# Optimization experiments

Hardware: AMD Instinct MI355X
Metric: run time of the kernel (lower is better)

The kernel has to match this reference:

```python
import jax, jax.numpy as jnp
import numpy as np

TAU = 1.2       # LIF membrane time constant
VTH = 0.5       # spike threshold
ALPHA = 4.0     # spikingjelly default sigmoid surrogate sharpness


def setup_inputs() -> dict:
    key = jax.random.key(0)
    ks = jax.random.split(key, 14)
    T, B, C, L = 4, 16, 256, 2048

    def lin_w(k, o, i):
        return (jax.random.normal(k, (o, i), jnp.float32) / np.sqrt(i)).astype(jnp.float32)

    def bias(k, o):
        return (jax.random.normal(k, (o,), jnp.float32) * 0.01).astype(jnp.float32)

    return {
        "x": jax.random.normal(ks[0], (T, B, C, L), jnp.float32),
        "diffusion_step": jax.random.randint(ks[1], (B,), 0, 50),
        # diffusion_embedding: Linear(1,C) -> SiLU -> Linear(C,C)
        "w_emb1": lin_w(ks[2], C, 1), "b_emb1": bias(ks[3], C),
        "w_emb2": lin_w(ks[4], C, C), "b_emb2": bias(ks[5], C),
        # diffusion_projection: Linear(C,C)
        "w_proj": lin_w(ks[6], C, C), "b_proj": bias(ks[7], C),
        # conv: Conv1d(C, 2C, k=3, pad=1)
        "w_conv": (jax.random.normal(ks[8], (2 * C, C, 3), jnp.float32) / np.sqrt(3 * C)).astype(jnp.float32),
        "b_conv": bias(ks[9], 2 * C),
        # skip_out / res_out: Conv1d(C, C, k=1)
        "w_skip": (jax.random.normal(ks[10], (C, C, 1), jnp.float32) / np.sqrt(C)).astype(jnp.float32),
        "b_skip": bias(ks[11], C),
        "w_res": (jax.random.normal(ks[12], (C, C, 1), jnp.float32) / np.sqrt(C)).astype(jnp.float32),
        "b_res": bias(ks[13], C),
    }


def _heaviside_surrogate(u):
    # forward: (u >= 0); backward: sigmoid surrogate (spikingjelly default)
    s = jax.nn.sigmoid(ALPHA * u)
    return s + jax.lax.stop_gradient((u >= 0).astype(u.dtype) - s)


def _lif_multistep(x_seq):
    # x_seq: (T, B, C2, L); hard reset to v_reset=0, detach_reset=True
    def step(v, xt):
        v = v + (xt - v) / TAU                      # decay_input charging
        spike = _heaviside_surrogate(v - VTH)
        v = v * (1.0 - jax.lax.stop_gradient(spike))  # detached hard reset
        return v, spike

    v0 = jnp.zeros(x_seq.shape[1:], x_seq.dtype)
    _, spikes = jax.lax.scan(step, v0, x_seq)
    return spikes


def reference(x, diffusion_step, w_emb1, b_emb1, w_emb2, b_emb2, w_proj, b_proj,
              w_conv, b_conv, w_skip, b_skip, w_res, b_res):
    T, B, C, L = x.shape
    ds = diffusion_step.reshape(B, 1).astype(jnp.float32)
    h = jax.nn.silu(ds @ w_emb1.T + b_emb1)           # (B, C)
    emb = h @ w_emb2.T + b_emb2                       # (B, C)
    proj = emb @ w_proj.T + b_proj                    # (B, C)

    y = x + proj[None, :, :, None]                    # broadcast over T, L

    # Conv1d over flattened (T*B) batch, C -> 2C, k=3, pad=1
    y2 = jax.lax.conv_general_dilated(
        y.reshape(T * B, C, L), w_conv, window_strides=(1,),
        padding=[(1, 1)], rhs_dilation=(1,),
        dimension_numbers=("NCH", "OIH", "NCH"))
    y2 = (y2 + b_conv[None, :, None]).reshape(T, B, 2 * C, L)

    spikes = _lif_multistep(y2)                       # (T, B, 2C, L) in {0,1}

    gate, filt = spikes[:, :, :C, :], spikes[:, :, C:, :]
    z = jax.nn.sigmoid(gate) * jnp.tanh(filt)         # (T, B, C, L)

    skip = jnp.einsum("tbcl,oc->tbol", z, w_skip[:, :, 0]) + b_skip[None, None, :, None]
    res = jnp.einsum("tbcl,oc->tbol", z, w_res[:, :, 0]) + b_res[None, None, :, None]
    return (x + res, skip)
```

## Files before the change

kernel.cpp:

```cpp
#include <hip/hip_runtime.h>
#include <hip/hip_bf16.h>


#define T_STEPS 4
#define BB 16
#define C_CH 256
#define O_CH 512
#define LL 2048
#define OUT_HALF 33554432

__global__ __launch_bounds__(256) void embed_proj_kernel(
    const int* __restrict__ dstep,
    const float* __restrict__ w_emb1, const float* __restrict__ b_emb1,
    const float* __restrict__ w_emb2, const float* __restrict__ b_emb2,
    const float* __restrict__ w_proj, const float* __restrict__ b_proj,
    const float* __restrict__ w_conv, const float* __restrict__ b_conv,
    float* __restrict__ pk)
{
    const int b = blockIdx.x;
    const int tid = threadIdx.x;
    __shared__ float h[256], emb[256], proj[256];
    const float ds = (float)dstep[b];
    {
        float t1 = ds * w_emb1[tid] + b_emb1[tid];
        float sg = 1.0f / (1.0f + expf(-t1));
        h[tid] = t1 * sg;
    }
    __syncthreads();
    {
        float s = b_emb2[tid];
        const float* wrow = w_emb2 + tid * 256;
        for (int c = 0; c < 256; ++c) s += h[c] * wrow[c];
        emb[tid] = s;
    }
    __syncthreads();
    {
        float s = b_proj[tid];
        const float* wrow = w_proj + tid * 256;
        for (int c = 0; c < 256; ++c) s += emb[c] * wrow[c];
        proj[tid] = s;
    }
    __syncthreads();
    for (int i = tid; i < 512 * 3; i += 256) {
        int o = i / 3, k = i - o * 3;
        float s = (k == 1) ? b_conv[o] : 0.0f;
        const float* wrow = w_conv + (size_t)o * 768 + k;
        for (int c = 0; c < 256; ++c) s += proj[c] * wrow[c * 3];
        pk[(size_t)b * 1536 + i] = s;
    }
}


#define XS_STRIDE 140

__device__ __forceinline__ void gll16(const float* g, float* l) {
    __builtin_amdgcn_global_load_lds(
        (const __attribute__((address_space(1))) void*)g,
        (__attribute__((address_space(3))) void*)l, 16, 0, 0);
}

__global__ __launch_bounds__(256, 2) void conv_lif_kernel(
    const float* __restrict__ x,
    const float* __restrict__ w_conv,
    const float* __restrict__ pk,
    __hip_bfloat16* __restrict__ zbuf)
{
    const int lb = blockIdx.x;
    const int ob = blockIdx.y;
    const int b  = blockIdx.z;
    const int l0 = lb * 128;
    const int g0 = ob * 64;
    const int tid = threadIdx.x;
    const int lg4 = (tid & 15) * 4;
    const int og8 = (tid >> 4) * 8;

    __shared__ float xs[32 * XS_STRIDE + 128];
    __shared__ float wsh[96 * 128];
    __shared__ float pksh[128 * 4];

    if (tid < 128) {
        int j = tid & 7, ogg = tid >> 3;
        int ch = g0 + ogg * 4 + (j & 3) + ((j & 4) ? 256 : 0);
        const float* p = pk + (size_t)b * 1536 + ch * 3;
        float p0 = p[0], p1 = p[1], p2 = p[2];
        pksh[tid * 4 + 0] = p0 + p1 + p2;
        pksh[tid * 4 + 1] = p0;
        pksh[tid * 4 + 2] = p2;
    }

    const int w_oo = tid >> 1;
    const int w_sub = tid & 1;
    const int w_j = w_oo & 7, w_og = w_oo >> 3;
    const int w_ch = g0 + w_og * 4 + (w_j & 3) + ((w_j & 4) ? 256 : 0);

    const float e0 = (lb == 0  && lg4 == 0)  ? 1.0f : 0.0f;
    const float e1 = (lb == 15 && lg4 == 60) ? 1.0f : 0.0f;

    float v[64];
#pragma unroll
    for (int i = 0; i < 64; ++i) v[i] = 0.0f;

    const float Z01 = 0.3807970780f;
    const float Z11 = 0.5567699413f;

    for (int t = 0; t < T_STEPS; ++t) {
        float acc[64];
#pragma unroll
        for (int i = 0; i < 64; ++i) acc[i] = 0.0f;

        const float* xsl = x + (size_t)(t * BB + b) * C_CH * LL;

        for (int cc = 0; cc < 8; ++cc) {
            __syncthreads();
            {
                const float* xc = xsl + (size_t)cc * 32 * LL;
#pragma unroll
                for (int r = 0; r < 4; ++r) {
                    int chunk = r * 256 + tid;
                    int row = chunk / 35;
                    int c16 = chunk - row * 35;
                    int off = l0 - 8 + c16 * 4;
                    off = (off < 0) ? 0 : ((off > LL - 4) ? (LL - 4) : off);
                    gll16(xc + (size_t)row * LL + off, &xs[chunk * 4]);
                }
                if (tid < 128) {
                    int chunk = 1024 + tid;
                    int row = chunk / 35;
                    int c16 = chunk - row * 35;
                    if (row > 31) { row = 31; }
                    int off = l0 - 8 + c16 * 4;
                    off = (off < 0) ? 0 : ((off > LL - 4) ? (LL - 4) : off);
                    gll16(xc + (size_t)row * LL + off, &xs[chunk * 4]);
                }
            }
            {
                const float* wsrc = w_conv + (size_t)w_ch * 768 + (cc * 32 + w_sub * 16) * 3;
                const int wb = w_sub * 48;
#pragma unroll
                for (int q = 0; q < 12; ++q) {
                    float4 w4 = *(const float4*)(wsrc + q * 4);
                    wsh[(wb + q * 4 + 0) * 128 + w_oo] = w4.x;
                    wsh[(wb + q * 4 + 1) * 128 + w_oo] = w4.y;
                    wsh[(wb + q * 4 + 2) * 128 + w_oo] = w4.z;
                    wsh[(wb + q * 4 + 3) * 128 + w_oo] = w4.w;
                }
            }
            __syncthreads();
            if (lb == 0) {
                if (tid < 32) xs[tid * XS_STRIDE + 7] = 0.0f;
                __syncthreads();
            } else if (lb == 15) {
                if (tid < 32) xs[tid * XS_STRIDE + 136] = 0.0f;
                __syncthreads();
            }
            for (int cl = 0; cl < 32; ++cl) {
                const int xb = cl * XS_STRIDE + lg4;
                float xw0[6], xw1[6];
                {
                    float4 xa = *(const float4*)&xs[xb + 8];
                    xw0[0] = xs[xb + 7];
                    xw0[1] = xa.x; xw0[2] = xa.y; xw0[3] = xa.z; xw0[4] = xa.w;
                    xw0[5] = xs[xb + 12];
                }
                {
                    float4 xa = *(const float4*)&xs[xb + 72];
                    xw1[0] = xs[xb + 71];
                    xw1[1] = xa.x; xw1[2] = xa.y; xw1[3] = xa.z; xw1[4] = xa.w;
                    xw1[5] = xs[xb + 76];
                }
#pragma unroll
                for (int k = 0; k < 3; ++k) {
                    float4 wa  = *(const float4*)&wsh[(cl * 3 + k) * 128 + og8];
                    float4 wb4 = *(const float4*)&wsh[(cl * 3 + k) * 128 + og8 + 4];
                    float wv[8] = { wa.x, wa.y, wa.z, wa.w, wb4.x, wb4.y, wb4.z, wb4.w };
#pragma unroll
                    for (int j = 0; j < 8; ++j) {
#pragma unroll
                        for (int lj = 0; lj < 4; ++lj) {
                            acc[j * 4 + lj]      += wv[j] * xw0[lj + k];
                            acc[32 + j * 4 + lj] += wv[j] * xw1[lj + k];
                        }
                    }
                }
            }
        }

#pragma unroll
        for (int g = 0; g < 2; ++g) {
#pragma unroll
            for (int j = 0; j < 8; ++j) {
                const int oo = og8 + j;
                const float psum = pksh[oo * 4 + 0];
#pragma unroll
                for (int lj = 0; lj < 4; ++lj) {
                    const int idx = g * 32 + j * 4 + lj;
                    float y2 = acc[idx] + psum;
                    if (g == 0 && lj == 0) y2 -= e0 * pksh[oo * 4 + 1];
                    if (g == 1 && lj == 3) y2 -= e1 * pksh[oo * 4 + 2];
                    float vv = v[idx];
                    vv = vv + (y2 - vv) / 1.2f;
                    float s = (vv >= 0.5f) ? 1.0f : 0.0f;
                    acc[idx] = s;
                    v[idx] = vv * (1.0f - s);
                }
            }
        }

#pragma unroll
        for (int g = 0; g < 2; ++g) {
#pragma unroll
            for (int jp = 0; jp < 4; ++jp) {
                union { __hip_bfloat16 h[4]; uint2 u; } pv;
#pragma unroll
                for (int lj = 0; lj < 4; ++lj) {
                    float gg = acc[g * 32 + jp * 4 + lj];
                    float ff = acc[g * 32 + (jp + 4) * 4 + lj];
                    float z = (ff != 0.0f) ? ((gg != 0.0f) ? Z11 : Z01) : 0.0f;
                    pv.h[lj] = __float2bfloat16(z);
                }
                int ch = g0 + (og8 >> 1) + jp;
                size_t zi = ((size_t)(t * BB + b) * C_CH + ch) * LL + l0 + g * 64 + lg4;
                *(uint2*)((char*)zbuf + zi * 2) = pv.u;
            }
        }
    }
}

__global__ __launch_bounds__(256) void out_gemm_kernel(
    const float* __restrict__ x,
    const __hip_bfloat16* __restrict__ zbuf,
    const float* __restrict__ w_skip, const float* __restrict__ b_skip,
    const float* __restrict__ w_res,  const float* __restrict__ b_res,
    float* __restrict__ out)
{
    const int lb  = blockIdx.x;
    const int obk = blockIdx.y;
    const int tb  = blockIdx.z;
    const int l0 = lb * 128, o0 = obk * 64;
    const int tid = threadIdx.x;
    const int lg = tid & 15, og = tid >> 4;

    __shared__ float zsh[32 * 132];
    __shared__ float wrh[32 * 68];
    __shared__ float wkh[32 * 68];

    float accR[32], accS[32];
#pragma unroll
    for (int i = 0; i < 32; ++i) { accR[i] = 0.0f; accS[i] = 0.0f; }

    const int z_row = tid >> 3;
    const int z_colg = tid & 7;

    for (int cc = 0; cc < 8; ++cc) {
        __syncthreads();
        {
            const __hip_bfloat16* zb = zbuf + ((size_t)tb * C_CH + cc * 32 + z_row) * LL
                                     + l0 + z_colg * 16;
#pragma unroll
            for (int half = 0; half < 2; ++half) {
                uint4 raw = *(const uint4*)((const char*)zb + half * 16);
                const unsigned int w[4] = { raw.x, raw.y, raw.z, raw.w };
                float f[8];
#pragma unroll
                for (int q = 0; q < 4; ++q) {
                    union { float fv; unsigned int uv; } lo, hi;
                    lo.uv = (w[q] & 0xFFFFu) << 16;
                    hi.uv = (w[q] & 0xFFFF0000u);
                    f[q * 2 + 0] = lo.fv;
                    f[q * 2 + 1] = hi.fv;
                }
                float4* dst = (float4*)&zsh[z_row * 132 + z_colg * 16 + half * 8];
                dst[0] = make_float4(f[0], f[1], f[2], f[3]);
                dst[1] = make_float4(f[4], f[5], f[6], f[7]);
            }
            for (int i = tid; i < 2048; i += 256) {
                int oo = i >> 5, cl = i & 31;
                int c = cc * 32 + cl;
                wrh[cl * 68 + oo] = w_res[(size_t)(o0 + oo) * 256 + c];
                wkh[cl * 68 + oo] = w_skip[(size_t)(o0 + oo) * 256 + c];
            }
        }
        __syncthreads();
        for (int cl = 0; cl < 32; ++cl) {
            float4 z0 = *(const float4*)&zsh[cl * 132 + lg * 4];
            float4 z1 = *(const float4*)&zsh[cl * 132 + 64 + lg * 4];
            float4 r4 = *(const float4*)&wrh[cl * 68 + og * 4];
            float4 k4 = *(const float4*)&wkh[cl * 68 + og * 4];
            float zz0[4] = { z0.x, z0.y, z0.z, z0.w };
            float zz1[4] = { z1.x, z1.y, z1.z, z1.w };
            float rr[4] = { r4.x, r4.y, r4.z, r4.w };
            float kk[4] = { k4.x, k4.y, k4.z, k4.w };
#pragma unroll
            for (int j = 0; j < 4; ++j) {
#pragma unroll
                for (int lj = 0; lj < 4; ++lj) {
                    accR[j * 4 + lj]      += rr[j] * zz0[lj];
                    accS[j * 4 + lj]      += kk[j] * zz0[lj];
                    accR[16 + j * 4 + lj] += rr[j] * zz1[lj];
                    accS[16 + j * 4 + lj] += kk[j] * zz1[lj];
                }
            }
        }
    }

    const size_t base = (size_t)tb * C_CH * LL;
#pragma unroll
    for (int g = 0; g < 2; ++g) {
#pragma unroll
        for (int j = 0; j < 4; ++j) {
            int o = o0 + og * 4 + j;
            float br = b_res[o], bs = b_skip[o];
            size_t idx = base + (size_t)o * LL + l0 + g * 64 + lg * 4;
            float4 x4 = *(const float4*)&x[idx];
            float4 ro, so;
            ro.x = x4.x + accR[g * 16 + j * 4 + 0] + br;
            ro.y = x4.y + accR[g * 16 + j * 4 + 1] + br;
            ro.z = x4.z + accR[g * 16 + j * 4 + 2] + br;
            ro.w = x4.w + accR[g * 16 + j * 4 + 3] + br;
            so.x = accS[g * 16 + j * 4 + 0] + bs;
            so.y = accS[g * 16 + j * 4 + 1] + bs;
            so.z = accS[g * 16 + j * 4 + 2] + bs;
            so.w = accS[g * 16 + j * 4 + 3] + bs;
            *(float4*)&out[idx] = ro;
            *(float4*)&out[OUT_HALF + idx] = so;
        }
    }
}

extern "C" void kernel_launch(void* const* d_in, const int* in_sizes, int n_in,
                              void* d_out, int out_size, void* d_ws, size_t ws_size,
                              hipStream_t stream) {
    const float* x       = (const float*)d_in[0];
    const int*   dstep   = (const int*)d_in[1];
    const float* w_emb1  = (const float*)d_in[2];
    const float* b_emb1  = (const float*)d_in[3];
    const float* w_emb2  = (const float*)d_in[4];
    const float* b_emb2  = (const float*)d_in[5];
    const float* w_proj  = (const float*)d_in[6];
    const float* b_proj  = (const float*)d_in[7];
    const float* w_conv  = (const float*)d_in[8];
    const float* b_conv  = (const float*)d_in[9];
    const float* w_skip  = (const float*)d_in[10];
    const float* b_skip  = (const float*)d_in[11];
    const float* w_res   = (const float*)d_in[12];
    const float* b_res   = (const float*)d_in[13];
    float* out = (float*)d_out;

    float* pk = (float*)d_ws;
    __hip_bfloat16* zbuf = (__hip_bfloat16*)((char*)d_ws + 131072);

    embed_proj_kernel<<<BB, 256, 0, stream>>>(dstep, w_emb1, b_emb1, w_emb2, b_emb2,
                                              w_proj, b_proj, w_conv, b_conv, pk);
    conv_lif_kernel<<<dim3(LL / 128, 4, BB), 256, 0, stream>>>(x, w_conv, pk, zbuf);
    out_gemm_kernel<<<dim3(LL / 128, C_CH / 64, T_STEPS * BB), 256, 0, stream>>>(
        x, zbuf, w_skip, b_skip, w_res, b_res, out);
}
```

Before: 1.985 ms.

## Use bf16 MFMA with split-precision weights for output GEMM and retile z layout

The 1x1 res/skip GEMM now runs on bf16 MFMA instructions. The weights are split into hi and lo bf16 parts to keep near-fp32 accuracy, and the z operand is read directly from global memory in a new K-blocked layout that conv_lif writes. The conv_lif kernel's channel chunk is halved to shrink shared memory so occupancy can rise to 4 blocks per SM. This trades scalar FMA work and LDS staging for matrix-core throughput. The costs are scalar, uncoalesced-per-lane output stores and doubled MFMA work for the lo correction.

Result: faster. 1.830 ms (-7.8%).

```diff
diff --git a/kernel.cpp b/kernel.cpp
--- a/kernel.cpp
+++ b/kernel.cpp
@@ -8,6 +8,9 @@
 #define O_CH 512
 #define LL 2048
 #define OUT_HALF 33554432
+
+typedef __bf16 bf16x8 __attribute__((ext_vector_type(8)));
+typedef float f32x4 __attribute__((ext_vector_type(4)));
 
 __global__ __launch_bounds__(256) void embed_proj_kernel(
     const int* __restrict__ dstep,
@@ -59,7 +62,7 @@
         (__attribute__((address_space(3))) void*)l, 16, 0, 0);
 }
 
-__global__ __launch_bounds__(256, 2) void conv_lif_kernel(
+__global__ __launch_bounds__(256, 4) void conv_lif_kernel(
     const float* __restrict__ x,
     const float* __restrict__ w_conv,
     const float* __restrict__ pk,
@@ -72,20 +75,21 @@
     const int g0 = ob * 64;
     const int tid = threadIdx.x;
     const int lg4 = (tid & 15) * 4;
-    const int og8 = (tid >> 4) * 8;
-
-    __shared__ float xs[32 * XS_STRIDE + 128];
-    __shared__ float wsh[96 * 128];
-    __shared__ float pksh[128 * 4];
+    const int og  = tid >> 4;
+    const int og8 = og * 8;
+
+    __shared__ float xs[16 * XS_STRIDE];
+    __shared__ float wsh[48 * 128];
+    __shared__ float pksh[128 * 3];
 
     if (tid < 128) {
         int j = tid & 7, ogg = tid >> 3;
         int ch = g0 + ogg * 4 + (j & 3) + ((j & 4) ? 256 : 0);
         const float* p = pk + (size_t)b * 1536 + ch * 3;
         float p0 = p[0], p1 = p[1], p2 = p[2];
-        pksh[tid * 4 + 0] = p0 + p1 + p2;
-        pksh[tid * 4 + 1] = p0;
-        pksh[tid * 4 + 2] = p2;
+        pksh[tid * 3 + 0] = p0 + p1 + p2;
+        pksh[tid * 3 + 1] = p0;
+        pksh[tid * 3 + 2] = p2;
     }
 
     const int w_oo = tid >> 1;
@@ -110,12 +114,12 @@
 
         const float* xsl = x + (size_t)(t * BB + b) * C_CH * LL;
 
-        for (int cc = 0; cc < 8; ++cc) {
+        for (int cc = 0; cc < 16; ++cc) {
             __syncthreads();
             {
-                const float* xc = xsl + (size_t)cc * 32 * LL;
-#pragma unroll
-                for (int r = 0; r < 4; ++r) {
+                const float* xc = xsl + (size_t)cc * 16 * LL;
+#pragma unroll
+                for (int r = 0; r < 2; ++r) {
                     int chunk = r * 256 + tid;
                     int row = chunk / 35;
                     int c16 = chunk - row * 35;
@@ -123,21 +127,20 @@
                     off = (off < 0) ? 0 : ((off > LL - 4) ? (LL - 4) : off);
                     gll16(xc + (size_t)row * LL + off, &xs[chunk * 4]);
                 }
-                if (tid < 128) {
-                    int chunk = 1024 + tid;
+                if (tid < 48) {
+                    int chunk = 512 + tid;
                     int row = chunk / 35;
                     int c16 = chunk - row * 35;
-                    if (row > 31) { row = 31; }
                     int off = l0 - 8 + c16 * 4;
                     off = (off < 0) ? 0 : ((off > LL - 4) ? (LL - 4) : off);
                     gll16(xc + (size_t)row * LL + off, &xs[chunk * 4]);
                 }
             }
             {
-                const float* wsrc = w_conv + (size_t)w_ch * 768 + (cc * 32 + w_sub * 16) * 3;
-                const int wb = w_sub * 48;
-#pragma unroll
-                for (int q = 0; q < 12; ++q) {
+                const float* wsrc = w_conv + (size_t)w_ch * 768 + (cc * 16 + w_sub * 8) * 3;
+                const int wb = w_sub * 24;
+#pragma unroll
+                for (int q = 0; q < 6; ++q) {
                     float4 w4 = *(const float4*)(wsrc + q * 4);
                     wsh[(wb + q * 4 + 0) * 128 + w_oo] = w4.x;
                     wsh[(wb + q * 4 + 1) * 128 + w_oo] = w4.y;
@@ -147,13 +150,13 @@
             }
             __syncthreads();
             if (lb == 0) {
-                if (tid < 32) xs[tid * XS_STRIDE + 7] = 0.0f;
+                if (tid < 16) xs[tid * XS_STRIDE + 7] = 0.0f;
                 __syncthreads();
             } else if (lb == 15) {
-                if (tid < 32) xs[tid * XS_STRIDE + 136] = 0.0f;
+                if (tid < 16) xs[tid * XS_STRIDE + 136] = 0.0f;
                 __syncthreads();
             }
-            for (int cl = 0; cl < 32; ++cl) {
+            for (int cl = 0; cl < 16; ++cl) {
                 const int xb = cl * XS_STRIDE + lg4;
                 float xw0[6], xw1[6];
                 {
@@ -190,13 +193,13 @@
 #pragma unroll
             for (int j = 0; j < 8; ++j) {
                 const int oo = og8 + j;
-                const float psum = pksh[oo * 4 + 0];
+                const float psum = pksh[oo * 3 + 0];
 #pragma unroll
                 for (int lj = 0; lj < 4; ++lj) {
                     const int idx = g * 32 + j * 4 + lj;
                     float y2 = acc[idx] + psum;
-                    if (g == 0 && lj == 0) y2 -= e0 * pksh[oo * 4 + 1];
-                    if (g == 1 && lj == 3) y2 -= e1 * pksh[oo * 4 + 2];
+                    if (g == 0 && lj == 0) y2 -= e0 * pksh[oo * 3 + 1];
+                    if (g == 1 && lj == 3) y2 -= e1 * pksh[oo * 3 + 2];
                     float vv = v[idx];
                     vv = vv + (y2 - vv) / 1.2f;
                     float s = (vv >= 0.5f) ? 1.0f : 0.0f;
@@ -206,27 +209,45 @@
             }
         }
 
-#pragma unroll
-        for (int g = 0; g < 2; ++g) {
-#pragma unroll
-            for (int jp = 0; jp < 4; ++jp) {
-                union { __hip_bfloat16 h[4]; uint2 u; } pv;
+        {
+            const int kkw = ob * 2 + (og >> 3);
+            const int ci0 = (og & 7) * 4;
+#pragma unroll
+            for (int g = 0; g < 2; ++g) {
 #pragma unroll
                 for (int lj = 0; lj < 4; ++lj) {
-                    float gg = acc[g * 32 + jp * 4 + lj];
-                    float ff = acc[g * 32 + (jp + 4) * 4 + lj];
-                    float z = (ff != 0.0f) ? ((gg != 0.0f) ? Z11 : Z01) : 0.0f;
-                    pv.h[lj] = __float2bfloat16(z);
-                }
-                int ch = g0 + (og8 >> 1) + jp;
-                size_t zi = ((size_t)(t * BB + b) * C_CH + ch) * LL + l0 + g * 64 + lg4;
-                *(uint2*)((char*)zbuf + zi * 2) = pv.u;
-            }
-        }
-    }
-}
-
-__global__ __launch_bounds__(256) void out_gemm_kernel(
+                    union { __hip_bfloat16 h[4]; uint2 u; } pv;
+#pragma unroll
+                    for (int jp = 0; jp < 4; ++jp) {
+                        float gg = acc[g * 32 + jp * 4 + lj];
+                        float ff = acc[g * 32 + (jp + 4) * 4 + lj];
+                        float z = (ff != 0.0f) ? ((gg != 0.0f) ? Z11 : Z01) : 0.0f;
+                        pv.h[jp] = __float2bfloat16(z);
+                    }
+                    int l = l0 + g * 64 + lg4 + lj;
+                    size_t zi = (((size_t)(t * BB + b) * 8 + kkw) * 2048 + l) * 32 + ci0;
+                    *(uint2*)((char*)zbuf + zi * 2) = pv.u;
+                }
+            }
+        }
+    }
+}
+
+__device__ __forceinline__ void make_afrag(const float* wp, bf16x8& hi, bf16x8& lo) {
+    float4 f0 = *(const float4*)wp;
+    float4 f1 = *(const float4*)(wp + 4);
+    float f[8] = { f0.x, f0.y, f0.z, f0.w, f1.x, f1.y, f1.z, f1.w };
+    union { __bf16 h[8]; bf16x8 v; } H, L;
+#pragma unroll
+    for (int i = 0; i < 8; ++i) {
+        __bf16 hv = (__bf16)f[i];
+        H.h[i] = hv;
+        L.h[i] = (__bf16)(f[i] - (float)hv);
+    }
+    hi = H.v; lo = L.v;
+}
+
+__global__ __launch_bounds__(256, 2) void out_gemm_kernel(
     const float* __restrict__ x,
     const __hip_bfloat16* __restrict__ zbuf,
     const float* __restrict__ w_skip, const float* __restrict__ b_skip,
@@ -238,91 +259,73 @@
     const int tb  = blockIdx.z;
     const int l0 = lb * 128, o0 = obk * 64;
     const int tid = threadIdx.x;
-    const int lg = tid & 15, og = tid >> 4;
-
-    __shared__ float zsh[32 * 132];
-    __shared__ float wrh[32 * 68];
-    __shared__ float wkh[32 * 68];
-
-    float accR[32], accS[32];
-#pragma unroll
-    for (int i = 0; i < 32; ++i) { accR[i] = 0.0f; accS[i] = 0.0f; }
-
-    const int z_row = tid >> 3;
-    const int z_colg = tid & 7;
-
-    for (int cc = 0; cc < 8; ++cc) {
-        __syncthreads();
-        {
-            const __hip_bfloat16* zb = zbuf + ((size_t)tb * C_CH + cc * 32 + z_row) * LL
-                                     + l0 + z_colg * 16;
-#pragma unroll
-            for (int half = 0; half < 2; ++half) {
-                uint4 raw = *(const uint4*)((const char*)zb + half * 16);
-                const unsigned int w[4] = { raw.x, raw.y, raw.z, raw.w };
-                float f[8];
-#pragma unroll
-                for (int q = 0; q < 4; ++q) {
-                    union { float fv; unsigned int uv; } lo, hi;
-                    lo.uv = (w[q] & 0xFFFFu) << 16;
-                    hi.uv = (w[q] & 0xFFFF0000u);
-                    f[q * 2 + 0] = lo.fv;
-                    f[q * 2 + 1] = hi.fv;
-                }
-                float4* dst = (float4*)&zsh[z_row * 132 + z_colg * 16 + half * 8];
-                dst[0] = make_float4(f[0], f[1], f[2], f[3]);
-                dst[1] = make_float4(f[4], f[5], f[6], f[7]);
-            }
-            for (int i = tid; i < 2048; i += 256) {
-                int oo = i >> 5, cl = i & 31;
-                int c = cc * 32 + cl;
-                wrh[cl * 68 + oo] = w_res[(size_t)(o0 + oo) * 256 + c];
-                wkh[cl * 68 + oo] = w_skip[(size_t)(o0 + oo) * 256 + c];
-            }
-        }
-        __syncthreads();
-        for (int cl = 0; cl < 32; ++cl) {
-            float4 z0 = *(const float4*)&zsh[cl * 132 + lg * 4];
-            float4 z1 = *(const float4*)&zsh[cl * 132 + 64 + lg * 4];
-            float4 r4 = *(const float4*)&wrh[cl * 68 + og * 4];
-            float4 k4 = *(const float4*)&wkh[cl * 68 + og * 4];
-            float zz0[4] = { z0.x, z0.y, z0.z, z0.w };
-            float zz1[4] = { z1.x, z1.y, z1.z, z1.w };
-            float rr[4] = { r4.x, r4.y, r4.z, r4.w };
-            float kk[4] = { k4.x, k4.y, k4.z, k4.w };
-#pragma unroll
-            for (int j = 0; j < 4; ++j) {
-#pragma unroll
-                for (int lj = 0; lj < 4; ++lj) {
-                    accR[j * 4 + lj]      += rr[j] * zz0[lj];
-                    accS[j * 4 + lj]      += kk[j] * zz0[lj];
-                    accR[16 + j * 4 + lj] += rr[j] * zz1[lj];
-                    accS[16 + j * 4 + lj] += kk[j] * zz1[lj];
-                }
+    const int lane = tid & 63;
+    const int wave = tid >> 6;
+    const int wo = wave & 1, wl = wave >> 1;
+    const int r16 = lane & 15;
+    const int kq  = lane >> 4;
+
+    const int obase = o0 + wo * 32;
+    const int lbase = l0 + wl * 64;
+
+    const f32x4 vzero = { 0.0f, 0.0f, 0.0f, 0.0f };
+    f32x4 accR[2][4], accS[2][4];
+#pragma unroll
+    for (int a = 0; a < 2; ++a)
+#pragma unroll
+        for (int c = 0; c < 4; ++c) { accR[a][c] = vzero; accS[a][c] = vzero; }
+
+    const char* zb = (const char*)zbuf
+        + (((size_t)tb * 8) * 2048 + (size_t)lbase + r16) * 64
+        + (size_t)kq * 16;
+    const float* wrp = w_res  + (size_t)(obase + r16) * 256 + kq * 8;
+    const float* wkp = w_skip + (size_t)(obase + r16) * 256 + kq * 8;
+
+#pragma unroll
+    for (int kk = 0; kk < 8; ++kk) {
+        bf16x8 Bv[4];
+#pragma unroll
+        for (int ls = 0; ls < 4; ++ls) {
+            union { uint4 u; bf16x8 v; } t2;
+            t2.u = *(const uint4*)(zb + (size_t)kk * (2048 * 64) + ls * (16 * 64));
+            Bv[ls] = t2.v;
+        }
+        bf16x8 AhR[2], AlR[2], AhS[2], AlS[2];
+#pragma unroll
+        for (int osub = 0; osub < 2; ++osub) {
+            make_afrag(wrp + osub * (16 * 256) + kk * 32, AhR[osub], AlR[osub]);
+            make_afrag(wkp + osub * (16 * 256) + kk * 32, AhS[osub], AlS[osub]);
+        }
+#pragma unroll
+        for (int osub = 0; osub < 2; ++osub) {
+#pragma unroll
+            for (int ls = 0; ls < 4; ++ls) {
+                accR[osub][ls] = __builtin_amdgcn_mfma_f32_16x16x32_bf16(
+                    AhR[osub], Bv[ls], accR[osub][ls], 0, 0, 0);
+                accR[osub][ls] = __builtin_amdgcn_mfma_f32_16x16x32_bf16(
+                    AlR[osub], Bv[ls], accR[osub][ls], 0, 0, 0);
+                accS[osub][ls] = __builtin_amdgcn_mfma_f32_16x16x32_bf16(
+                    AhS[osub], Bv[ls], accS[osub][ls], 0, 0, 0);
+                accS[osub][ls] = __builtin_amdgcn_mfma_f32_16x16x32_bf16(
+                    AlS[osub], Bv[ls], accS[osub][ls], 0, 0, 0);
             }
         }
     }
 
     const size_t base = (size_t)tb * C_CH * LL;
 #pragma unroll
-    for (int g = 0; g < 2; ++g) {
-#pragma unroll
-        for (int j = 0; j < 4; ++j) {
-            int o = o0 + og * 4 + j;
-            float br = b_res[o], bs = b_skip[o];
-            size_t idx = base + (size_t)o * LL + l0 + g * 64 + lg * 4;
-            float4 x4 = *(const float4*)&x[idx];
-            float4 ro, so;
-            ro.x = x4.x + accR[g * 16 + j * 4 + 0] + br;
-            ro.y = x4.y + accR[g * 16 + j * 4 + 1] + br;
-            ro.z = x4.z + accR[g * 16 + j * 4 + 2] + br;
-            ro.w = x4.w + accR[g * 16 + j * 4 + 3] + br;
-            so.x = accS[g * 16 + j * 4 + 0] + bs;
-            so.y = accS[g * 16 + j * 4 + 1] + bs;
-            so.z = accS[g * 16 + j * 4 + 2] + bs;
-            so.w = accS[g * 16 + j * 4 + 3] + bs;
-            *(float4*)&out[idx] = ro;
-            *(float4*)&out[OUT_HALF + idx] = so;
+    for (int osub = 0; osub < 2; ++osub) {
+#pragma unroll
+        for (int r = 0; r < 4; ++r) {
+            const int o = obase + osub * 16 + kq * 4 + r;
+            const float br = b_res[o], bs = b_skip[o];
+#pragma unroll
+            for (int ls = 0; ls < 4; ++ls) {
+                const int l = lbase + ls * 16 + r16;
+                const size_t idx = base + (size_t)o * LL + l;
+                out[idx] = x[idx] + accR[osub][ls][r] + br;
+                out[OUT_HALF + idx] = accS[osub][ls][r] + bs;
+            }
         }
     }
 }
```
